# Kernel tuning notes

Measured on AMD Instinct MI355X. Metric: run time of the kernel, lower is better.

The kernel has to match this reference:

```python
import jax, jax.numpy as jnp
import numpy as np

N_HEAD = 16
D_MODEL = 1024
D_HEAD = D_MODEL // N_HEAD
B, T = 2, 2048


def setup_inputs() -> dict:
    key = jax.random.key(0)
    k1, k2, k3 = jax.random.split(key, 3)
    x = jax.random.normal(k1, (B, T, D_MODEL), dtype=jnp.float32)
    w_attn = jax.random.normal(k2, (3 * D_MODEL, D_MODEL), dtype=jnp.float32) * (D_MODEL ** -0.5)
    w_proj = jax.random.normal(k3, (D_MODEL, D_MODEL), dtype=jnp.float32) * (D_MODEL ** -0.5)
    return {"x": x, "w_attn": w_attn, "w_proj": w_proj}


def _rms_norm(x):
    eps = jnp.asarray(jnp.finfo(x.dtype).eps, x.dtype)
    var = jnp.mean(jnp.square(x), axis=-1, keepdims=True)
    return x * jax.lax.rsqrt(var + eps)


def _rotate_half(x):
    x1, x2 = jnp.split(x, 2, axis=-1)
    return jnp.concatenate((-x2, x1), axis=-1)


def reference(x, w_attn, w_proj):
    Bx, Tx, C = x.shape
    qkv = jnp.einsum('btc,fc->btf', x, w_attn)  # [B,T,3C]
    q, k, v = jnp.split(qkv, 3, axis=-1)
    # [B, H, T, Dh]
    q = q.reshape(Bx, Tx, N_HEAD, D_HEAD).transpose(0, 2, 1, 3)
    k = k.reshape(Bx, Tx, N_HEAD, D_HEAD).transpose(0, 2, 1, 3)
    v = v.reshape(Bx, Tx, N_HEAD, D_HEAD).transpose(0, 2, 1, 3)
    # QK RMSNorm (no learned weight)
    q = _rms_norm(q)
    k = _rms_norm(k)
    # Rotary embedding over full d_head: freqs tiled twice
    inv_freq = 1.0 / (10000.0 ** (jnp.arange(0, D_HEAD, 2, dtype=jnp.float32) / D_HEAD))
    t = jnp.arange(Tx, dtype=jnp.float32)
    freqs = jnp.einsum('i,j->ij', t, inv_freq)  # [T, Dh/2]
    emb = jnp.concatenate((freqs, freqs), axis=-1)  # [T, Dh]
    cos = jnp.cos(emb)[None, None, :, :]
    sin = jnp.sin(emb)[None, None, :, :]
    q = q * cos + _rotate_half(q) * sin
    k = k * cos + _rotate_half(k) * sin
    # Causal SDPA
    scale = D_HEAD ** -0.5
    scores = jnp.einsum('bhqd,bhkd->bhqk', q, k) * scale
    causal = jnp.tril(jnp.ones((Tx, Tx), dtype=bool))
    scores = jnp.where(causal[None, None], scores, jnp.asarray(-jnp.inf, scores.dtype))
    attn = jax.nn.softmax(scores, axis=-1)
    y = jnp.einsum('bhqk,bhkd->bhqd', attn, v)
    y = y.transpose(0, 2, 1, 3).reshape(Bx, Tx, C)
    return jnp.einsum('btc,oc->bto', y, w_proj)
```

## Files before the change

### kernel.cpp

```cpp
#include <hip/hip_runtime.h>
#include <cstdint>
#include <cstddef>


typedef short bf16x8 __attribute__((ext_vector_type(8)));
typedef float floatx4 __attribute__((ext_vector_type(4)));
typedef float floatx2 __attribute__((ext_vector_type(2)));
typedef unsigned short ushortx8 __attribute__((ext_vector_type(8)));
typedef unsigned short ushortx4 __attribute__((ext_vector_type(4)));
typedef unsigned int uintx2 __attribute__((ext_vector_type(2)));

#define DEVI __device__ __forceinline__

DEVI float bf2f(unsigned short u) {
    unsigned int x = ((unsigned int)u) << 16;
    return __builtin_bit_cast(float, x);
}
DEVI unsigned short f2bf(float f) {
    unsigned int u = __builtin_bit_cast(unsigned int, f);
    u += 0x7fffu + ((u >> 16) & 1u);
    return (unsigned short)(u >> 16);
}
DEVI unsigned int pkbf2(float a, float b) {
    unsigned int ua = __builtin_bit_cast(unsigned int, a) + 0x8000u;
    unsigned int ub = __builtin_bit_cast(unsigned int, b) + 0x8000u;
    return __builtin_amdgcn_perm(ub, ua, 0x07060302);
}

DEVI void glds16(const unsigned short* g, unsigned short* l) {
    __builtin_amdgcn_global_load_lds(
        (const __attribute__((address_space(1))) unsigned int*)g,
        (__attribute__((address_space(3))) unsigned int*)l, 16, 0, 0);
}

DEVI void cast8(unsigned short* dst, const float* src) {
    floatx4 a = *(const floatx4*)src;
    floatx4 b = *(const floatx4*)(src + 4);
    ushortx8 o;
    o[0] = f2bf(a[0]); o[1] = f2bf(a[1]); o[2] = f2bf(a[2]); o[3] = f2bf(a[3]);
    o[4] = f2bf(b[0]); o[5] = f2bf(b[1]); o[6] = f2bf(b[2]); o[7] = f2bf(b[3]);
    *(ushortx8*)dst = o;
}

__global__ __launch_bounds__(256)
void cast_inputs(const float* __restrict__ x, const float* __restrict__ wa,
                 const float* __restrict__ wp,
                 unsigned short* __restrict__ xb, unsigned short* __restrict__ wab,
                 unsigned short* __restrict__ wpb, float* __restrict__ ropetab)
{
    size_t g = (size_t)blockIdx.x * 256 + threadIdx.x;
    size_t stride = (size_t)gridDim.x * 256;
    for (size_t i = g; i < (4194304 / 8); i += stride) cast8(xb  + i * 8, x  + i * 8);
    for (size_t i = g; i < (3145728 / 8); i += stride) cast8(wab + i * 8, wa + i * 8);
    for (size_t i = g; i < (1048576 / 8); i += stride) cast8(wpb + i * 8, wp + i * 8);
    for (size_t i = g; i < 65536; i += stride) {
        int t = (int)(i >> 5), f = (int)(i & 31);
        float ang = (float)t * __expf(-(float)f * 0.28782313662425572f);
        float sn, cs;
        __sincosf(ang, &sn, &cs);
        ropetab[2 * i]     = cs;
        ropetab[2 * i + 1] = sn;
    }
}

__global__ __launch_bounds__(512, 2)
void gemm_qkv_8ph(const unsigned short* __restrict__ A,
                  const unsigned short* __restrict__ B,
                  const float* __restrict__ ropetab,
                  unsigned short* __restrict__ Cqk,
                  unsigned short* __restrict__ Vt)
{
    __shared__ __align__(16) unsigned short lds[2][2][256 * 64];

    const int tid  = threadIdx.x;
    const int lane = tid & 63;
    const int w    = tid >> 6;
    const int wm   = w >> 2;
    const int wn   = w & 3;
    const int quad = lane >> 4;
    const int lm   = lane & 15;

    const int lin = blockIdx.y * 12 + blockIdx.x;
    const int s   = (lin & 7) * 24 + (lin >> 3);
    const int m0  = (s / 12) * 256;
    const int n0  = (s % 12) * 256;

    const int srow = tid >> 3;
    const int scol = (((tid & 7) ^ ((tid >> 3) & 7)) * 8);
    const int ldst = w * 512;

#define STG_A(u, WBi, kq) glds16(&A[(size_t)(m0 + (u) * 64 + srow) * 1024 + (kq) + scol], \
                                 &lds[WBi][0][(u) * 4096 + ldst])
#define STG_B(u, WBi, kq) glds16(&B[(size_t)(n0 + (u) * 64 + srow) * 1024 + (kq) + scol], \
                                 &lds[WBi][1][(u) * 4096 + ldst])
#define RD_A(RBi, rrow, kk) (*(const bf16x8*)&lds[RBi][0][(rrow) * 64 + ((((kk) * 4 + quad) ^ ((rrow) & 7)) * 8)])
#define RD_B(RBi, rrow, kk) (*(const bf16x8*)&lds[RBi][1][(rrow) * 64 + ((((kk) * 4 + quad) ^ ((rrow) & 7)) * 8)])

    floatx4 acc[8][4] = {};
    bf16x8 afr[4][2];
    bf16x8 bfr[4][2];

#define MQ(MB, JB)                                                              \
  do {                                                                          \
    _Pragma("unroll")                                                           \
    for (int kk = 0; kk < 2; ++kk)                                              \
      _Pragma("unroll")                                                         \
      for (int mi = 0; mi < 4; ++mi)                                            \
        _Pragma("unroll")                                                       \
        for (int j2 = 0; j2 < 2; ++j2)                                          \
          acc[(MB) + mi][(JB) + j2] = __builtin_amdgcn_mfma_f32_16x16x32_bf16(  \
              afr[mi][kk], bfr[(JB) + j2][kk], acc[(MB) + mi][(JB) + j2], 0, 0, 0); \
  } while (0)

#define TILE(RBi, WBi, KT, LASTF)                                               \
  do {                                                                          \
    const int kn = ((KT) + 1) * 64;                                             \
    if (!(LASTF)) { STG_B(0, WBi, kn); STG_B(1, WBi, kn); }                     \
    _Pragma("unroll")                                                           \
    for (int kk = 0; kk < 2; ++kk) {                                            \
      _Pragma("unroll")                                                         \
      for (int mi = 0; mi < 4; ++mi)                                            \
        afr[mi][kk] = RD_A(RBi, wm * 128 + mi * 16 + lm, kk);                   \
      _Pragma("unroll")                                                         \
      for (int j2 = 0; j2 < 2; ++j2)                                            \
        bfr[j2][kk] = RD_B(RBi, wn * 64 + j2 * 16 + lm, kk);                    \
    }                                                                           \
    asm volatile("s_waitcnt lgkmcnt(8)" ::: "memory");                          \
    __builtin_amdgcn_s_barrier();                                               \
    asm volatile("s_waitcnt lgkmcnt(0)" ::: "memory");                          \
    __builtin_amdgcn_s_setprio(1); MQ(0, 0); __builtin_amdgcn_s_setprio(0);     \
    __builtin_amdgcn_s_barrier();                                               \
    if (!(LASTF)) { STG_B(2, WBi, kn); STG_B(3, WBi, kn); }                     \
    _Pragma("unroll")                                                           \
    for (int kk = 0; kk < 2; ++kk)                                              \
      _Pragma("unroll")                                                         \
      for (int j2 = 0; j2 < 2; ++j2)                                            \
        bfr[2 + j2][kk] = RD_B(RBi, wn * 64 + (2 + j2) * 16 + lm, kk);          \
    if (!(LASTF)) { asm volatile("s_waitcnt vmcnt(4)" ::: "memory"); }          \
    else          { asm volatile("s_waitcnt vmcnt(0)" ::: "memory"); }          \
    __builtin_amdgcn_s_barrier();                                               \
    asm volatile("s_waitcnt lgkmcnt(0)" ::: "memory");                          \
    __builtin_amdgcn_s_setprio(1); MQ(0, 2); __builtin_amdgcn_s_setprio(0);     \
    __builtin_amdgcn_s_barrier();                                               \
    if (!(LASTF)) { STG_A(0, WBi, kn); STG_A(2, WBi, kn); }                     \
    _Pragma("unroll")                                                           \
    for (int kk = 0; kk < 2; ++kk)                                              \
      _Pragma("unroll")                                                         \
      for (int mi = 0; mi < 4; ++mi)                                            \
        afr[mi][kk] = RD_A(RBi, wm * 128 + 64 + mi * 16 + lm, kk);              \
    __builtin_amdgcn_s_barrier();                                               \
    asm volatile("s_waitcnt lgkmcnt(0)" ::: "memory");                          \
    __builtin_amdgcn_s_setprio(1); MQ(4, 2); __builtin_amdgcn_s_setprio(0);     \
    __builtin_amdgcn_s_barrier();                                               \
    if (!(LASTF)) { STG_A(1, WBi, kn); STG_A(3, WBi, kn);                       \
                    asm volatile("s_waitcnt vmcnt(2)" ::: "memory"); }          \
    __builtin_amdgcn_s_barrier();                                               \
    __builtin_amdgcn_s_setprio(1); MQ(4, 0); __builtin_amdgcn_s_setprio(0);     \
    __builtin_amdgcn_s_barrier();                                               \
  } while (0)

    STG_B(0, 0, 0); STG_B(1, 0, 0); STG_B(2, 0, 0); STG_B(3, 0, 0);
    STG_A(0, 0, 0); STG_A(2, 0, 0); STG_A(1, 0, 0); STG_A(3, 0, 0);
    asm volatile("s_waitcnt vmcnt(2)" ::: "memory");
    __builtin_amdgcn_s_barrier();

    for (int kt = 0; kt < 14; kt += 2) {
        TILE(0, 1, kt, false);
        TILE(1, 0, kt + 1, false);
    }
    TILE(0, 1, 14, false);
    TILE(1, 0, 15, true);

    const bool is_v = (n0 + wn * 64) >= 2048;
    if (!is_v) {
        const floatx2* rtab = (const floatx2*)ropetab;
        #pragma unroll
        for (int mi = 0; mi < 8; ++mi) {
            float rn[4];
            #pragma unroll
            for (int r = 0; r < 4; ++r) {
                float ss = 0.0f;
                #pragma unroll
                for (int j = 0; j < 4; ++j) ss += acc[mi][j][r] * acc[mi][j][r];
                ss += __shfl_xor(ss, 1, 64);
                ss += __shfl_xor(ss, 2, 64);
                ss += __shfl_xor(ss, 4, 64);
                ss += __shfl_xor(ss, 8, 64);
                rn[r] = rsqrtf(ss * (1.0f / 64.0f) + 1.1920929e-07f);
            }
            #pragma unroll
            for (int r = 0; r < 4; ++r) {
                int row = m0 + wm * 128 + mi * 16 + quad * 4 + r;
                int t = row & 2047;
                floatx2 cs0 = rtab[t * 32 + lm];
                floatx2 cs1 = rtab[t * 32 + 16 + lm];
                float g = rn[r];
                #pragma unroll
                for (int j = 0; j < 4; ++j) {
                    int d = j * 16 + lm;
                    float cs = (j & 1) ? cs1[0] : cs0[0];
                    float sn = (j & 1) ? cs1[1] : cs0[1];
                    float v  = acc[mi][j][r] * g;
                    float vp = acc[mi][j ^ 2][r] * g;
                    float sgn = (d < 32) ? -1.0f : 1.0f;
                    Cqk[(size_t)row * 2048 + (n0 + wn * 64 + d)] =
                        f2bf(v * cs + sgn * vp * sn);
                }
            }
        }
    } else {
        #pragma unroll
        for (int mi = 0; mi < 8; ++mi)
            #pragma unroll
            for (int j = 0; j < 4; ++j) {
                int col  = n0 + wn * 64 + j * 16 + lm;
                int row0 = m0 + wm * 128 + mi * 16 + quad * 4;
                int bq = row0 >> 11, t0 = row0 & 2047;
                ushortx4 pk;
                #pragma unroll
                for (int r = 0; r < 4; ++r) pk[r] = f2bf(acc[mi][j][r]);
                *(ushortx4*)&Vt[((size_t)(bq * 1024 + (col - 2048))) * 2048 + t0] = pk;
            }
    }
#undef TILE
#undef MQ
#undef RD_A
#undef RD_B
#undef STG_A
#undef STG_B
}

template <int BN, int BK>
__global__ __launch_bounds__(256)
void gemm_bt(const unsigned short* __restrict__ A, const unsigned short* __restrict__ B,
             float* __restrict__ Cf, int M, int N, int K)
{
    constexpr int WCOLS = (BN == 128) ? 2 : 1;
    constexpr int WROWS = 4 / WCOLS;
    constexpr int MI    = 128 / (16 * WROWS);
    constexpr int LPR   = BK / 8;
    constexpr int RPI   = 64 / LPR;

    __shared__ __align__(16) unsigned short As[128 * BK];
    __shared__ __align__(16) unsigned short Bs[BN * BK];

    const int tid  = threadIdx.x;
    const int lane = tid & 63;
    const int w    = tid >> 6;
    const int wm   = w / WCOLS, wn = w % WCOLS;
    const int quad = lane >> 4;
    const int lm   = lane & 15;
    const int m0 = blockIdx.y * 128;
    const int n0 = blockIdx.x * BN;
    const int sr = lane / LPR;
    const int sc = (lane % LPR) * 8;

    floatx4 acc[MI][4] = {};

    for (int k0 = 0; k0 < K; k0 += BK) {
        __syncthreads();
        #pragma unroll
        for (int i = 0; i < 32 / RPI; ++i) {
            int r = w * 32 + i * RPI;
            glds16(&A[(size_t)(m0 + r + sr) * K + k0 + sc], &As[r * BK]);
        }
        #pragma unroll
        for (int i = 0; i < (BN / 4) / RPI; ++i) {
            int r = w * (BN / 4) + i * RPI;
            glds16(&B[(size_t)(n0 + r + sr) * K + k0 + sc], &Bs[r * BK]);
        }
        __syncthreads();

        #pragma unroll
        for (int kk = 0; kk < BK / 32; ++kk) {
            bf16x8 a[MI];
            #pragma unroll
            for (int i = 0; i < MI; ++i)
                a[i] = *(const bf16x8*)&As[(wm * (16 * MI) + i * 16 + lm) * BK + kk * 32 + quad * 8];
            #pragma unroll
            for (int j = 0; j < 4; ++j) {
                bf16x8 b = *(const bf16x8*)&Bs[(wn * 64 + j * 16 + lm) * BK + kk * 32 + quad * 8];
                #pragma unroll
                for (int i = 0; i < MI; ++i)
                    acc[i][j] = __builtin_amdgcn_mfma_f32_16x16x32_bf16(a[i], b, acc[i][j], 0, 0, 0);
            }
        }
    }

    #pragma unroll
    for (int i = 0; i < MI; ++i)
        #pragma unroll
        for (int j = 0; j < 4; ++j) {
            int col  = n0 + wn * 64 + j * 16 + lm;
            int row0 = m0 + wm * (16 * MI) + i * 16 + quad * 4;
            #pragma unroll
            for (int r = 0; r < 4; ++r)
                Cf[(size_t)(row0 + r) * N + col] = acc[i][j][r];
        }
}

#define ENC(qt, t0, nt) ((qt) | ((t0) << 8) | ((nt) << 16))
__constant__ int g_items[24] = {
    ENC(15,16,16), ENC(15,0,16), ENC(14,0,16), ENC(13,0,16), ENC(12,0,16),
    ENC(11,0,16),  ENC(10,0,16), ENC(9,0,16),  ENC(8,0,16),  ENC(7,0,16),
    ENC(14,16,14), ENC(6,0,14),  ENC(13,16,12), ENC(5,0,12),
    ENC(12,16,10), ENC(4,0,10),  ENC(11,16,8),  ENC(3,0,8),
    ENC(10,16,6),  ENC(2,0,6),   ENC(9,16,4),   ENC(1,0,4),
    ENC(8,16,2),   ENC(0,0,2)
};

#define ATTN_EXP(SA, QROW, PROW, KT, DG)                                       \
  do {                                                                         \
    _Pragma("unroll")                                                          \
    for (int j = 0; j < 4; ++j) {                                              \
      float p0 = exp2f((SA)[j][0] * c1 - c2);                                  \
      float p1 = exp2f((SA)[j][1] * c1 - c2);                                  \
      float p2 = exp2f((SA)[j][2] * c1 - c2);                                  \
      float p3 = exp2f((SA)[j][3] * c1 - c2);                                  \
      if (DG) {                                                                \
        int kb = (KT) * 64 + j * 16 + quad * 4;                                \
        if (kb + 0 > (QROW)) p0 = 0.0f;                                        \
        if (kb + 1 > (QROW)) p1 = 0.0f;                                        \
        if (kb + 2 > (QROW)) p2 = 0.0f;                                        \
        if (kb + 3 > (QROW)) p3 = 0.0f;                                        \
      }                                                                        \
      uintx2 pk;                                                               \
      pk[0] = pkbf2(p0, p1);                                                   \
      pk[1] = pkbf2(p2, p3);                                                   \
      *(uintx2*)&QPs[(PROW) * 64 + (((2 * j + (quad >> 1)) ^ sx) * 8) + (quad & 1) * 4] = pk; \
    }                                                                          \
  } while (0)

#define ATTN_STEP(KSc, VSc, KSn, VSn, KT, DG, LAST)                            \
  do {                                                                         \
    if (!(LAST)) {                                                             \
      *(ushortx8*)&(KSn)[wkA] = kregA; *(ushortx8*)&(KSn)[wkB] = kregB;        \
      *(ushortx8*)&(VSn)[wkA] = vregA; *(ushortx8*)&(VSn)[wkB] = vregB;        \
      if ((KT) + 2 <= lastk) {                                                 \
        kregA = *(const ushortx8*)kpA; kregB = *(const ushortx8*)kpB;          \
        vregA = *(const ushortx8*)vpA; vregB = *(const ushortx8*)vpB;          \
        kpA += (size_t)64 * 2048; kpB += (size_t)64 * 2048;                    \
        vpA += 64; vpB += 64;                                                  \
      }                                                                        \
    }                                                                          \
    floatx4 sa0[4] = {}, sa1[4] = {};                                          \
    _Pragma("unroll")                                                          \
    for (int kk = 0; kk < 2; ++kk)                                             \
      _Pragma("unroll")                                                        \
      for (int j = 0; j < 4; ++j) {                                            \
        bf16x8 kf = *(const bf16x8*)&(KSc)[(j * 16 + lm) * 64 + (((kk * 4 + quad) ^ sx) * 8)]; \
        sa0[j] = __builtin_amdgcn_mfma_f32_16x16x32_bf16(kf, qf0[kk], sa0[j], 0, 0, 0); \
        sa1[j] = __builtin_amdgcn_mfma_f32_16x16x32_bf16(kf, qf1[kk], sa1[j], 0, 0, 0); \
      }                                                                        \
    ATTN_EXP(sa0, qrow0, w * 32 + lm,      KT, DG);                            \
    ATTN_EXP(sa1, qrow1, w * 32 + 16 + lm, KT, DG);                            \
    _Pragma("unroll")                                                          \
    for (int kk = 0; kk < 2; ++kk) {                                           \
      bf16x8 pf0 = *(const bf16x8*)&QPs[(w * 32 + lm) * 64 + (((kk * 4 + quad) ^ sx) * 8)]; \
      bf16x8 pf1 = *(const bf16x8*)&QPs[(w * 32 + 16 + lm) * 64 + (((kk * 4 + quad) ^ sx) * 8)]; \
      _Pragma("unroll")                                                        \
      for (int j = 0; j < 4; ++j) {                                            \
        bf16x8 vf = *(const bf16x8*)&(VSc)[(j * 16 + lm) * 64 + (((kk * 4 + quad) ^ sx) * 8)]; \
        o0[j] = __builtin_amdgcn_mfma_f32_16x16x32_bf16(pf0, vf, o0[j], 0, 0, 0); \
        o1[j] = __builtin_amdgcn_mfma_f32_16x16x32_bf16(pf1, vf, o1[j], 0, 0, 0); \
      }                                                                        \
      l0 = __builtin_amdgcn_mfma_f32_16x16x32_bf16(pf0, ones, l0, 0, 0, 0);    \
      l1 = __builtin_amdgcn_mfma_f32_16x16x32_bf16(pf1, ones, l1, 0, 0, 0);    \
    }                                                                          \
    if (!(LAST)) __syncthreads();                                              \
  } while (0)

__global__ __launch_bounds__(256, 3)
void attention(const unsigned short* __restrict__ qk,
               const unsigned short* __restrict__ Vt,
               unsigned short* __restrict__ Y,
               float* __restrict__ Po, float* __restrict__ Pl)
{
    __shared__ __align__(16) unsigned short QPs[128 * 64];
    __shared__ __align__(16) unsigned short Ks0[64 * 64];
    __shared__ __align__(16) unsigned short Ks1[64 * 64];
    __shared__ __align__(16) unsigned short Vs0[64 * 64];
    __shared__ __align__(16) unsigned short Vs1[64 * 64];

    const int tid  = threadIdx.x;
    const int lane = tid & 63;
    const int w    = tid >> 6;
    const int quad = lane >> 4;
    const int lm   = lane & 15;
    const int sx   = lm & 7;

    const int bh = blockIdx.x;
    const int it = g_items[blockIdx.y];
    const int qt = it & 255;
    const int t0 = (it >> 8) & 255;
    const int nt = it >> 16;
    const int b  = bh >> 4, h = bh & 15;
    const int q0 = qt * 128;
    const int qrow0 = q0 + w * 32 + lm;
    const int qrow1 = qrow0 + 16;
    const int lastk = t0 + nt - 1;
    const bool mflag = (t0 + nt) == (2 * qt + 2);
    const bool partial = qt >= 8;

    const int sr  = tid >> 3;
    const int sch = tid & 7;
    const int swz = ((sch ^ (sr & 7)) * 8);
    const int wkA = sr * 64 + swz;
    const int wkB = (sr + 32) * 64 + swz;

    const unsigned short* kpA = qk + (size_t)b * 2048 * 2048 + 1024 + h * 64
                              + (size_t)(t0 * 64 + sr) * 2048 + sch * 8;
    const unsigned short* kpB = kpA + (size_t)32 * 2048;
    const unsigned short* vpA = Vt + (size_t)bh * 64 * 2048 + (size_t)sr * 2048
                              + t0 * 64 + sch * 8;
    const unsigned short* vpB = vpA + (size_t)32 * 2048;

    #pragma unroll
    for (int p = 0; p < 4; ++p) {
        int row = p * 32 + sr;
        *(ushortx8*)&QPs[row * 64 + swz] =
            *(const ushortx8*)&qk[((size_t)(b * 2048 + q0 + row)) * 2048 + h * 64 + sch * 8];
    }

    ushortx8 kregA = *(const ushortx8*)kpA, kregB = *(const ushortx8*)kpB;
    ushortx8 vregA = *(const ushortx8*)vpA, vregB = *(const ushortx8*)vpB;
    kpA += (size_t)64 * 2048; kpB += (size_t)64 * 2048; vpA += 64; vpB += 64;
    *(ushortx8*)&Ks0[wkA] = kregA; *(ushortx8*)&Ks0[wkB] = kregB;
    *(ushortx8*)&Vs0[wkA] = vregA; *(ushortx8*)&Vs0[wkB] = vregB;
    kregA = *(const ushortx8*)kpA; kregB = *(const ushortx8*)kpB;
    vregA = *(const ushortx8*)vpA; vregB = *(const ushortx8*)vpB;
    kpA += (size_t)64 * 2048; kpB += (size_t)64 * 2048; vpA += 64; vpB += 64;
    __syncthreads();

    bf16x8 qf0[2], qf1[2];
    #pragma unroll
    for (int kk = 0; kk < 2; ++kk) {
        qf0[kk] = *(const bf16x8*)&QPs[(w * 32 + lm) * 64 + (((kk * 4 + quad) ^ sx) * 8)];
        qf1[kk] = *(const bf16x8*)&QPs[(w * 32 + 16 + lm) * 64 + (((kk * 4 + quad) ^ sx) * 8)];
    }

    bf16x8 ones;
    #pragma unroll
    for (int i = 0; i < 8; ++i) ones[i] = (short)0x3F80;

    floatx4 o0[4] = {}, o1[4] = {};
    floatx4 l0 = {}, l1 = {};
    const float c1 = 0.125f * 1.44269504f;
    const float c2 = 8.0f   * 1.44269504f;

    int ct = 0;
    for (; ct + 3 < nt; ct += 2) {
        ATTN_STEP(Ks0, Vs0, Ks1, Vs1, t0 + ct,     false, false);
        ATTN_STEP(Ks1, Vs1, Ks0, Vs0, t0 + ct + 1, false, false);
    }
    ATTN_STEP(Ks0, Vs0, Ks1, Vs1, t0 + ct,     mflag, false);
    ATTN_STEP(Ks1, Vs1, Ks0, Vs0, t0 + ct + 1, mflag, true);

    if (!partial) {
        float rinv0[4], rinv1[4];
        #pragma unroll
        for (int r = 0; r < 4; ++r) { rinv0[r] = 1.0f / l0[r]; rinv1[r] = 1.0f / l1[r]; }
        #pragma unroll
        for (int j = 0; j < 4; ++j) {
            int colg = h * 64 + j * 16 + lm;
            #pragma unroll
            for (int r = 0; r < 4; ++r) {
                int rowg0 = q0 + w * 32 + quad * 4 + r;
                Y[((size_t)(b * 2048 + rowg0)) * 1024 + colg] = f2bf(o0[j][r] * rinv0[r]);
                Y[((size_t)(b * 2048 + rowg0 + 16)) * 1024 + colg] = f2bf(o1[j][r] * rinv1[r]);
            }
        }
    } else {
        const int pidx = (bh * 8 + (qt - 8)) * 2 + (t0 ? 1 : 0);
        float* po = Po + (size_t)pidx * 8192;
        #pragma unroll
        for (int j = 0; j < 4; ++j)
            #pragma unroll
            for (int r = 0; r < 4; ++r) {
                int row0 = w * 32 + quad * 4 + r;
                po[row0 * 64 + j * 16 + lm]        = o0[j][r];
                po[(row0 + 16) * 64 + j * 16 + lm] = o1[j][r];
            }
        if (lm == 0) {
            float* pl = Pl + (size_t)pidx * 128;
            #pragma unroll
            for (int r = 0; r < 4; ++r) {
                pl[w * 32 + quad * 4 + r]      = l0[r];
                pl[w * 32 + 16 + quad * 4 + r] = l1[r];
            }
        }
    }
}

__global__ __launch_bounds__(256)
void attn_reduce(const float* __restrict__ Po, const float* __restrict__ Pl,
                 unsigned short* __restrict__ Y)
{
    const int bh = blockIdx.x, qi = blockIdx.y;
    const int b = bh >> 4, h = bh & 15;
    const int q0 = (8 + qi) * 128;
    const int tid = threadIdx.x;
    const int row = tid >> 1;
    const int c0  = (tid & 1) * 32;
    const size_t base = ((size_t)(bh * 8 + qi)) * 2;
    const float* po0 = Po + (base + 0) * 8192 + row * 64 + c0;
    const float* po1 = Po + (base + 1) * 8192 + row * 64 + c0;
    const float rinv = 1.0f / (Pl[(base + 0) * 128 + row] + Pl[(base + 1) * 128 + row]);
    unsigned short* yp = Y + ((size_t)(b * 2048 + q0 + row)) * 1024 + h * 64 + c0;
    #pragma unroll
    for (int c = 0; c < 4; ++c) {
        floatx4 a  = *(const floatx4*)(po0 + c * 8);
        floatx4 a2 = *(const floatx4*)(po0 + c * 8 + 4);
        floatx4 e  = *(const floatx4*)(po1 + c * 8);
        floatx4 e2 = *(const floatx4*)(po1 + c * 8 + 4);
        ushortx8 o;
        o[0] = f2bf((a[0]  + e[0])  * rinv);
        o[1] = f2bf((a[1]  + e[1])  * rinv);
        o[2] = f2bf((a[2]  + e[2])  * rinv);
        o[3] = f2bf((a[3]  + e[3])  * rinv);
        o[4] = f2bf((a2[0] + e2[0]) * rinv);
        o[5] = f2bf((a2[1] + e2[1]) * rinv);
        o[6] = f2bf((a2[2] + e2[2]) * rinv);
        o[7] = f2bf((a2[3] + e2[3]) * rinv);
        *(ushortx8*)(yp + c * 8) = o;
    }
}

extern "C" void kernel_launch(void* const* d_in, const int* in_sizes, int n_in,
                              void* d_out, int out_size, void* d_ws, size_t ws_size,
                              hipStream_t stream)
{
    const float* x      = (const float*)d_in[0];
    const float* w_attn = (const float*)d_in[1];
    const float* w_proj = (const float*)d_in[2];
    float* out = (float*)d_out;

    unsigned short* qkbuf = (unsigned short*)d_ws;
    unsigned short* Vtb   = qkbuf + (size_t)4096 * 2048;
    unsigned short* y     = Vtb   + (size_t)32 * 64 * 2048;
    unsigned short* wpb   = y     + (size_t)4096 * 1024;
    float* Plb            = (float*)(wpb + (size_t)1024 * 1024);
    unsigned short* xb  = (unsigned short*)d_out;
    unsigned short* wab = xb + (size_t)4096 * 1024;
    float* ropetab = (float*)(wab + (size_t)3072 * 1024);
    float* Pob = (float*)d_out;

    dim3 blk(256);
    cast_inputs<<<dim3(1024), blk, 0, stream>>>(x, w_attn, w_proj, xb, wab, wpb, ropetab);
    gemm_qkv_8ph<<<dim3(12, 16), dim3(512), 0, stream>>>(xb, wab, ropetab, qkbuf, Vtb);
    attention<<<dim3(32, 24), blk, 0, stream>>>(qkbuf, Vtb, y, Pob, Plb);
    attn_reduce<<<dim3(32, 8), blk, 0, stream>>>(Pob, Plb, y);
    gemm_bt<64, 64>
        <<<dim3(16, 32), blk, 0, stream>>>(y, wpb, out, 4096, 1024, 1024);
}
```

Measured before the change: 181.0 us.

## Load K/V MFMA fragments directly from global memory, dropping LDS staging

Removes the double-buffered shared-memory staging of K and V tiles and the per-step __syncthreads. Each wave now loads its K and V MFMA operand fragments straight from global memory into registers. This cuts LDS traffic, barriers and LDS footprint, which may allow more occupancy. In exchange each of the 4 waves re-reads the same K/V tile from global/L2 (4x redundant loads), uses strided 16-byte accesses, and no longer prefetches a tile ahead, so load latency is exposed.

Measured after the change: 220.9 us. +22.0%, slower.

```diff
diff --git a/kernel.cpp b/kernel.cpp
--- a/kernel.cpp
+++ b/kernel.cpp
@@ -331,27 +331,30 @@
     }                                                                          \
   } while (0)
 
-#define ATTN_STEP(KSc, VSc, KSn, VSn, KT, DG, LAST)                            \
+#define ATTN_STEP_G(KT, DG)                                                    \
   do {                                                                         \
-    if (!(LAST)) {                                                             \
-      *(ushortx8*)&(KSn)[wkA] = kregA; *(ushortx8*)&(KSn)[wkB] = kregB;        \
-      *(ushortx8*)&(VSn)[wkA] = vregA; *(ushortx8*)&(VSn)[wkB] = vregB;        \
-      if ((KT) + 2 <= lastk) {                                                 \
-        kregA = *(const ushortx8*)kpA; kregB = *(const ushortx8*)kpB;          \
-        vregA = *(const ushortx8*)vpA; vregB = *(const ushortx8*)vpB;          \
-        kpA += (size_t)64 * 2048; kpB += (size_t)64 * 2048;                    \
-        vpA += 64; vpB += 64;                                                  \
-      }                                                                        \
-    }                                                                          \
+    const unsigned short* kro = kbase + (size_t)(KT) * 64 * 2048;              \
+    const unsigned short* vco = vbase + (KT) * 64;                             \
+    bf16x8 kfr[2][4];                                                          \
+    _Pragma("unroll")                                                          \
+    for (int kk = 0; kk < 2; ++kk)                                             \
+      _Pragma("unroll")                                                        \
+      for (int j = 0; j < 4; ++j)                                              \
+        kfr[kk][j] = *(const bf16x8*)&kro[(size_t)(j * 16 + lm) * 2048 + kk * 32 + quad * 8]; \
     floatx4 sa0[4] = {}, sa1[4] = {};                                          \
     _Pragma("unroll")                                                          \
     for (int kk = 0; kk < 2; ++kk)                                             \
       _Pragma("unroll")                                                        \
       for (int j = 0; j < 4; ++j) {                                            \
-        bf16x8 kf = *(const bf16x8*)&(KSc)[(j * 16 + lm) * 64 + (((kk * 4 + quad) ^ sx) * 8)]; \
-        sa0[j] = __builtin_amdgcn_mfma_f32_16x16x32_bf16(kf, qf0[kk], sa0[j], 0, 0, 0); \
-        sa1[j] = __builtin_amdgcn_mfma_f32_16x16x32_bf16(kf, qf1[kk], sa1[j], 0, 0, 0); \
+        sa0[j] = __builtin_amdgcn_mfma_f32_16x16x32_bf16(kfr[kk][j], qf0[kk], sa0[j], 0, 0, 0); \
+        sa1[j] = __builtin_amdgcn_mfma_f32_16x16x32_bf16(kfr[kk][j], qf1[kk], sa1[j], 0, 0, 0); \
       }                                                                        \
+    bf16x8 vfr[2][4];                                                          \
+    _Pragma("unroll")                                                          \
+    for (int kk = 0; kk < 2; ++kk)                                             \
+      _Pragma("unroll")                                                        \
+      for (int j = 0; j < 4; ++j)                                              \
+        vfr[kk][j] = *(const bf16x8*)&vco[(size_t)(j * 16 + lm) * 2048 + kk * 32 + quad * 8]; \
     ATTN_EXP(sa0, qrow0, w * 32 + lm,      KT, DG);                            \
     ATTN_EXP(sa1, qrow1, w * 32 + 16 + lm, KT, DG);                            \
     _Pragma("unroll")                                                          \
@@ -360,14 +363,12 @@
       bf16x8 pf1 = *(const bf16x8*)&QPs[(w * 32 + 16 + lm) * 64 + (((kk * 4 + quad) ^ sx) * 8)]; \
       _Pragma("unroll")                                                        \
       for (int j = 0; j < 4; ++j) {                                            \
-        bf16x8 vf = *(const bf16x8*)&(VSc)[(j * 16 + lm) * 64 + (((kk * 4 + quad) ^ sx) * 8)]; \
-        o0[j] = __builtin_amdgcn_mfma_f32_16x16x32_bf16(pf0, vf, o0[j], 0, 0, 0); \
-        o1[j] = __builtin_amdgcn_mfma_f32_16x16x32_bf16(pf1, vf, o1[j], 0, 0, 0); \
+        o0[j] = __builtin_amdgcn_mfma_f32_16x16x32_bf16(pf0, vfr[kk][j], o0[j], 0, 0, 0); \
+        o1[j] = __builtin_amdgcn_mfma_f32_16x16x32_bf16(pf1, vfr[kk][j], o1[j], 0, 0, 0); \
       }                                                                        \
       l0 = __builtin_amdgcn_mfma_f32_16x16x32_bf16(pf0, ones, l0, 0, 0, 0);    \
       l1 = __builtin_amdgcn_mfma_f32_16x16x32_bf16(pf1, ones, l1, 0, 0, 0);    \
     }                                                                          \
-    if (!(LAST)) __syncthreads();                                              \
   } while (0)
 
 __global__ __launch_bounds__(256, 3)
@@ -377,10 +378,6 @@
                float* __restrict__ Po, float* __restrict__ Pl)
 {
     __shared__ __align__(16) unsigned short QPs[128 * 64];
-    __shared__ __align__(16) unsigned short Ks0[64 * 64];
-    __shared__ __align__(16) unsigned short Ks1[64 * 64];
-    __shared__ __align__(16) unsigned short Vs0[64 * 64];
-    __shared__ __align__(16) unsigned short Vs1[64 * 64];
 
     const int tid  = threadIdx.x;
     const int lane = tid & 63;
@@ -398,22 +395,15 @@
     const int q0 = qt * 128;
     const int qrow0 = q0 + w * 32 + lm;
     const int qrow1 = qrow0 + 16;
-    const int lastk = t0 + nt - 1;
     const bool mflag = (t0 + nt) == (2 * qt + 2);
     const bool partial = qt >= 8;
 
     const int sr  = tid >> 3;
     const int sch = tid & 7;
     const int swz = ((sch ^ (sr & 7)) * 8);
-    const int wkA = sr * 64 + swz;
-    const int wkB = (sr + 32) * 64 + swz;
-
-    const unsigned short* kpA = qk + (size_t)b * 2048 * 2048 + 1024 + h * 64
-                              + (size_t)(t0 * 64 + sr) * 2048 + sch * 8;
-    const unsigned short* kpB = kpA + (size_t)32 * 2048;
-    const unsigned short* vpA = Vt + (size_t)bh * 64 * 2048 + (size_t)sr * 2048
-                              + t0 * 64 + sch * 8;
-    const unsigned short* vpB = vpA + (size_t)32 * 2048;
+
+    const unsigned short* kbase = qk + (size_t)b * 2048 * 2048 + 1024 + h * 64;
+    const unsigned short* vbase = Vt + (size_t)bh * 64 * 2048;
 
     #pragma unroll
     for (int p = 0; p < 4; ++p) {
@@ -421,15 +411,6 @@
         *(ushortx8*)&QPs[row * 64 + swz] =
             *(const ushortx8*)&qk[((size_t)(b * 2048 + q0 + row)) * 2048 + h * 64 + sch * 8];
     }
-
-    ushortx8 kregA = *(const ushortx8*)kpA, kregB = *(const ushortx8*)kpB;
-    ushortx8 vregA = *(const ushortx8*)vpA, vregB = *(const ushortx8*)vpB;
-    kpA += (size_t)64 * 2048; kpB += (size_t)64 * 2048; vpA += 64; vpB += 64;
-    *(ushortx8*)&Ks0[wkA] = kregA; *(ushortx8*)&Ks0[wkB] = kregB;
-    *(ushortx8*)&Vs0[wkA] = vregA; *(ushortx8*)&Vs0[wkB] = vregB;
-    kregA = *(const ushortx8*)kpA; kregB = *(const ushortx8*)kpB;
-    vregA = *(const ushortx8*)vpA; vregB = *(const ushortx8*)vpB;
-    kpA += (size_t)64 * 2048; kpB += (size_t)64 * 2048; vpA += 64; vpB += 64;
     __syncthreads();
 
     bf16x8 qf0[2], qf1[2];
@@ -448,13 +429,10 @@
     const float c1 = 0.125f * 1.44269504f;
     const float c2 = 8.0f   * 1.44269504f;
 
+    const int nm = mflag ? nt - 2 : nt;
     int ct = 0;
-    for (; ct + 3 < nt; ct += 2) {
-        ATTN_STEP(Ks0, Vs0, Ks1, Vs1, t0 + ct,     false, false);
-        ATTN_STEP(Ks1, Vs1, Ks0, Vs0, t0 + ct + 1, false, false);
-    }
-    ATTN_STEP(Ks0, Vs0, Ks1, Vs1, t0 + ct,     mflag, false);
-    ATTN_STEP(Ks1, Vs1, Ks0, Vs0, t0 + ct + 1, mflag, true);
+    for (; ct < nm; ++ct) ATTN_STEP_G(t0 + ct, false);
+    for (; ct < nt; ++ct) ATTN_STEP_G(t0 + ct, true);
 
     if (!partial) {
         float rinv0[4], rinv1[4];
```
